# Optimization experiments

Hardware: AMD Instinct MI355X
Metric: run time of the kernel (lower is better)

The kernel has to match this reference:

```python
import jax, jax.numpy as jnp
import numpy as np

B, T, D, H, E = 4, 2048, 1024, 1024, 8
NEG_SLOPE = 0.01  # torch LeakyReLU default

def leaky_relu(x):
    return jnp.where(x >= 0, x, NEG_SLOPE * x)

def setup_inputs() -> dict:
    key = jax.random.key(0)
    ks = jax.random.split(key, 10)
    s = 0.02
    return {
        "x": jax.random.normal(ks[0], (B, T, D), jnp.float32),
        "gate_w": jax.random.normal(ks[1], (D, E), jnp.float32) * s,
        "gate_b": jnp.zeros((E,), jnp.float32),
        "w1": jax.random.normal(ks[2], (E, D, H), jnp.float32) * s,
        "b1": jnp.zeros((E, H), jnp.float32),
        "w2": jax.random.normal(ks[3], (E, H, H), jnp.float32) * s,
        "b2": jnp.zeros((E, H), jnp.float32),
        "w3": jax.random.normal(ks[4], (E, H, D), jnp.float32) * s,
        "b3": jnp.zeros((E, D), jnp.float32),
        "topn": 2,
    }

def reference(x, gate_w, gate_b, w1, b1, w2, b2, w3, b3, topn):
    # Gating: softmax over experts, top-k mask, L1 renormalize
    gating = jax.nn.softmax(x @ gate_w + gate_b, axis=-1)          # [B,T,E]
    _, topk_idx = jax.lax.top_k(gating, topn)                       # [B,T,k]
    mask = jax.nn.one_hot(topk_idx, E, dtype=gating.dtype).sum(-2)  # [B,T,E]
    g = gating * mask
    g = g / jnp.maximum(jnp.sum(jnp.abs(g), axis=-1, keepdims=True), 1e-12)
    # Dense all-expert MLP: Linear -> LeakyReLU -> Linear -> LeakyReLU -> Linear
    h = leaky_relu(jnp.einsum('btd,edh->bteh', x, w1) + b1)         # [B,T,E,H]
    h = leaky_relu(jnp.einsum('bteh,ehg->bteg', h, w2) + b2)        # [B,T,E,H]
    eo = jnp.einsum('bteh,ehd->bted', h, w3) + b3                   # [B,T,E,D]
    # Weighted combine
    return jnp.einsum('bte,bted->btd', g, eo)                       # [B,T,D]
```

## Files before the change

kernel.cpp:

```cpp
#include <hip/hip_runtime.h>
#include <hip/hip_bf16.h>
#include <stdint.h>

#define TOKENS   8192
#define DDIM     1024
#define EXPERTS  8
#define NSLOT    (TOKENS * 2)
#define MAXTILE  136

typedef __bf16 bf16x8_t __attribute__((ext_vector_type(8)));
typedef __bf16 bf16x4_t __attribute__((ext_vector_type(4)));
typedef float  f32x4_t  __attribute__((ext_vector_type(4)));

__device__ __forceinline__ void gl_lds16(const void* g, void* l) {
  __builtin_amdgcn_global_load_lds(
      (const __attribute__((address_space(1))) void*)g,
      (__attribute__((address_space(3))) void*)l, 16, 0, 0);
}

__global__ void twt_k(const float* __restrict__ w1, const float* __restrict__ w2,
                      const float* __restrict__ w3, __bf16* __restrict__ w1T,
                      __bf16* __restrict__ w2T, __bf16* __restrict__ w3T) {
  __shared__ float tile[64][33];
  const int layer = blockIdx.z >> 3, e = blockIdx.z & 7;
  const float* w = (layer == 0) ? w1 : (layer == 1) ? w2 : w3;
  __bf16* wT = (layer == 0) ? w1T : (layer == 1) ? w2T : w3T;
  const int kb = blockIdx.x * 64, nb = blockIdx.y * 32;
  const size_t ebase = (size_t)e << 20;
  const int tx = threadIdx.x, ty = threadIdx.y;
  const float* src = w + ebase;
#pragma unroll
  for (int r = ty; r < 64; r += 8)
    tile[r][tx] = src[(size_t)(kb + r) * 1024 + nb + tx];
  __syncthreads();
  __bf16* dst = wT + ebase;
#pragma unroll
  for (int r = ty; r < 32; r += 8) {
    union { __bf16 h[2]; unsigned u; } pk;
    pk.h[0] = (__bf16)tile[2 * tx][r];
    pk.h[1] = (__bf16)tile[2 * tx + 1][r];
    *(unsigned*)(dst + (size_t)(nb + r) * 1024 + kb + 2 * tx) = pk.u;
  }
}

__global__ __launch_bounds__(256) void gate_k(
    const float* __restrict__ x, const float* __restrict__ gw,
    const float* __restrict__ gb, __bf16* __restrict__ xbf,
    int* __restrict__ top_i, float* __restrict__ top_w) {
  const int t = blockIdx.x * 4 + (threadIdx.x >> 6);
  const int lane = threadIdx.x & 63;
  const float4* x4 = (const float4*)(x + (size_t)t * DDIM);
  bf16x4_t* xo4 = (bf16x4_t*)(xbf + (size_t)t * DDIM);
  const float4* g4 = (const float4*)gw;
  float acc[EXPERTS];
#pragma unroll
  for (int e = 0; e < EXPERTS; ++e) acc[e] = 0.f;
#pragma unroll
  for (int d4 = lane; d4 < 256; d4 += 64) {
    const float4 v = x4[d4];
    bf16x4_t o = {(__bf16)v.x, (__bf16)v.y, (__bf16)v.z, (__bf16)v.w};
    xo4[d4] = o;
    const float4* g = g4 + (size_t)d4 * 8;
    float4 ga, gbv;
    ga = g[0]; gbv = g[1];
    acc[0] += v.x * ga.x; acc[1] += v.x * ga.y; acc[2] += v.x * ga.z; acc[3] += v.x * ga.w;
    acc[4] += v.x * gbv.x; acc[5] += v.x * gbv.y; acc[6] += v.x * gbv.z; acc[7] += v.x * gbv.w;
    ga = g[2]; gbv = g[3];
    acc[0] += v.y * ga.x; acc[1] += v.y * ga.y; acc[2] += v.y * ga.z; acc[3] += v.y * ga.w;
    acc[4] += v.y * gbv.x; acc[5] += v.y * gbv.y; acc[6] += v.y * gbv.z; acc[7] += v.y * gbv.w;
    ga = g[4]; gbv = g[5];
    acc[0] += v.z * ga.x; acc[1] += v.z * ga.y; acc[2] += v.z * ga.z; acc[3] += v.z * ga.w;
    acc[4] += v.z * gbv.x; acc[5] += v.z * gbv.y; acc[6] += v.z * gbv.z; acc[7] += v.z * gbv.w;
    ga = g[6]; gbv = g[7];
    acc[0] += v.w * ga.x; acc[1] += v.w * ga.y; acc[2] += v.w * ga.z; acc[3] += v.w * ga.w;
    acc[4] += v.w * gbv.x; acc[5] += v.w * gbv.y; acc[6] += v.w * gbv.z; acc[7] += v.w * gbv.w;
  }
#pragma unroll
  for (int e = 0; e < EXPERTS; ++e)
    for (int s = 32; s > 0; s >>= 1) acc[e] += __shfl_down(acc[e], s);
  if (lane == 0) {
#pragma unroll
    for (int e = 0; e < EXPERTS; ++e) acc[e] += gb[e];
    int i1 = 0;
    for (int e = 1; e < EXPERTS; ++e)
      if (acc[e] > acc[i1]) i1 = e;
    int i2 = (i1 == 0) ? 1 : 0;
    for (int e = 0; e < EXPERTS; ++e)
      if (e != i1 && acc[e] > acc[i2]) i2 = e;
    const float r = expf(acc[i2] - acc[i1]);
    const float wA = 1.f / (1.f + r);
    const float wB = r / (1.f + r);
    top_i[t * 2] = i1; top_i[t * 2 + 1] = i2;
    top_w[t * 2] = wA; top_w[t * 2 + 1] = wB;
  }
}

__global__ __launch_bounds__(1024) void plan_k(
    const int* __restrict__ top_i, int* __restrict__ eoff,
    int* __restrict__ tok_list, int* __restrict__ slot_of,
    int4* __restrict__ work, int* __restrict__ ntiles) {
  const int tid = threadIdx.x;
  const int lane = tid & 63, wid = tid >> 6;
  __shared__ int ws[16][EXPERTS];
  __shared__ int eoff_s[EXPERTS];
  __shared__ int base_lds[1024 * EXPERTS];

  int ids[16];
  unsigned long long h64 = 0;
#pragma unroll
  for (int j = 0; j < 16; ++j) {
    ids[j] = top_i[tid * 16 + j];
    h64 += 1ull << (ids[j] * 8);
  }
#pragma unroll
  for (int e = 0; e < EXPERTS; ++e) {
    const int h = (int)((h64 >> (8 * e)) & 0xff);
    int v = h;
    for (int s = 1; s < 64; s <<= 1) {
      const int u = __shfl_up(v, s);
      if (lane >= s) v += u;
    }
    const int excl = v - h;
    const int tot = __shfl(v, 63);
    if (lane == 0) ws[wid][e] = tot;
    base_lds[tid * EXPERTS + e] = excl;
  }
  __syncthreads();
  if (tid == 0) {
    int tot[EXPERTS];
    for (int e = 0; e < EXPERTS; ++e) {
      int run = 0;
      for (int w = 0; w < 16; ++w) { const int c = ws[w][e]; ws[w][e] = run; run += c; }
      tot[e] = run;
    }
    int s = 0, nt = 0;
    for (int e = 0; e < EXPERTS; ++e) {
      const int te = tot[e];
      eoff_s[e] = s; eoff[e] = s;
      const int mt = (te + 127) >> 7;
      for (int i = 0; i < mt; ++i) { work[nt] = make_int4(e, i << 7, s, te); ++nt; }
      s += te;
    }
    eoff[EXPERTS] = s;
    ntiles[0] = nt;
  }
  __syncthreads();
#pragma unroll
  for (int e = 0; e < EXPERTS; ++e)
    base_lds[tid * EXPERTS + e] += eoff_s[e] + ws[wid][e];
  unsigned long long pre64 = 0;
#pragma unroll
  for (int j = 0; j < 16; ++j) {
    const int entry = tid * 16 + j;
    const int e = ids[j];
    const int pre = (int)((pre64 >> (8 * e)) & 0xff);
    pre64 += 1ull << (8 * e);
    const int s = base_lds[tid * EXPERTS + e] + pre;
    tok_list[s] = entry >> 1;
    slot_of[entry] = s;
  }
}

template <int GATHER, int LEAKY>
__global__ __launch_bounds__(256) void moe_gemm(
    const __bf16* __restrict__ A, const int* __restrict__ tok,
    const __bf16* __restrict__ W, const float* __restrict__ bias,
    const int4* __restrict__ work, const int* __restrict__ ntiles,
    __bf16* __restrict__ out) {
  if ((int)blockIdx.y >= ntiles[0]) return;
  const int4 wk = work[blockIdx.y];
  const int e = wk.x;
  const int m0 = wk.y;
  const int off = wk.z;
  const int ne = wk.w;
  const int n0 = blockIdx.x * 128;

  __shared__ __align__(16) __bf16 As[3][128 * 32];
  __shared__ __align__(16) __bf16 Bs[3][128 * 32];

  const int tid = threadIdx.x;
  const int lane = tid & 63;
  const int wid = tid >> 6;
  const int wm = wid >> 1, wn = wid & 1;
  const int ln = lane & 15, quad = lane >> 4;

  const __bf16* aptr[2];
  const __bf16* bptr[2];
#pragma unroll
  for (int j = 0; j < 2; ++j) {
    const int c = (wid * 2 + j) * 64 + lane;
    const int row = c >> 2;
    const int kc = (c & 3) ^ ((row >> 1) & 3);
    int r = m0 + row;
    if (r >= ne) r = m0;
    const long arow = GATHER ? (long)tok[off + r] : (long)(off + r);
    aptr[j] = A + arow * DDIM + kc * 8;
    bptr[j] = W + ((long)e << 20) + (long)(n0 + row) * 1024 + kc * 8;
  }
  const int st0 = (wid * 2) * 512;
  const int st1 = (wid * 2 + 1) * 512;

  const int swz = (quad ^ ((ln >> 1) & 3)) * 8;

  const f32x4_t vzero = {0.f, 0.f, 0.f, 0.f};
  f32x4_t acc[4][4];
#pragma unroll
  for (int i = 0; i < 4; ++i)
#pragma unroll
    for (int j = 0; j < 4; ++j) acc[i][j] = vzero;

#define STAGE(SB, KT)                                        \
  do {                                                       \
    const int k0_ = (KT) * 32;                               \
    gl_lds16(aptr[0] + k0_, (__bf16*)As[SB] + st0);          \
    gl_lds16(aptr[1] + k0_, (__bf16*)As[SB] + st1);          \
    gl_lds16(bptr[0] + k0_, (__bf16*)Bs[SB] + st0);          \
    gl_lds16(bptr[1] + k0_, (__bf16*)Bs[SB] + st1);          \
  } while (0)

#define WAITB(N)                                             \
  do {                                                       \
    asm volatile("s_waitcnt vmcnt(" #N ")" ::: "memory");    \
    __builtin_amdgcn_s_barrier();                            \
  } while (0)

#define COMPUTE(CUR)                                                        \
  do {                                                                      \
    bf16x8_t aF[4], bF[4];                                                  \
    _Pragma("unroll") for (int i = 0; i < 4; ++i)                           \
        aF[i] = *(const bf16x8_t*)(&As[CUR][(wm * 64 + i * 16 + ln) * 32 +  \
                                            swz]);                          \
    _Pragma("unroll") for (int j = 0; j < 4; ++j)                           \
        bF[j] = *(const bf16x8_t*)(&Bs[CUR][(wn * 64 + j * 16 + ln) * 32 +  \
                                            swz]);                          \
    _Pragma("unroll") for (int i = 0; i < 4; ++i)                           \
        _Pragma("unroll") for (int j = 0; j < 4; ++j)                       \
            acc[i][j] = __builtin_amdgcn_mfma_f32_16x16x32_bf16(            \
                bF[j], aF[i], acc[i][j], 0, 0, 0);                          \
  } while (0)

  STAGE(0, 0);
  STAGE(1, 1);

#pragma unroll 1
  for (int kt = 0; kt < 30; kt += 3) {
    WAITB(4); STAGE(2, kt + 2); COMPUTE(0);
    WAITB(4); STAGE(0, kt + 3); COMPUTE(1);
    WAITB(4); STAGE(1, kt + 4); COMPUTE(2);
  }
  WAITB(4); COMPUTE(0);
  WAITB(0); COMPUTE(1);

#undef STAGE
#undef WAITB
#undef COMPUTE

  const float* bs = bias + (e << 10);
  const int nb = n0 + wn * 64 + quad * 4;
  float4 bv[4];
#pragma unroll
  for (int j = 0; j < 4; ++j) bv[j] = *(const float4*)(bs + nb + j * 16);
#pragma unroll
  for (int i = 0; i < 4; ++i) {
    const int m = m0 + wm * 64 + i * 16 + ln;
    if (m < ne) {
      __bf16* orow = out + (size_t)(off + m) * 1024 + nb;
#pragma unroll
      for (int j = 0; j < 4; ++j) {
        float t0 = acc[i][j][0] + bv[j].x;
        float t1 = acc[i][j][1] + bv[j].y;
        float t2 = acc[i][j][2] + bv[j].z;
        float t3 = acc[i][j][3] + bv[j].w;
        if (LEAKY) {
          t0 = (t0 >= 0.f) ? t0 : 0.01f * t0;
          t1 = (t1 >= 0.f) ? t1 : 0.01f * t1;
          t2 = (t2 >= 0.f) ? t2 : 0.01f * t2;
          t3 = (t3 >= 0.f) ? t3 : 0.01f * t3;
        }
        bf16x4_t pk = {(__bf16)t0, (__bf16)t1, (__bf16)t2, (__bf16)t3};
        *(bf16x4_t*)(orow + j * 16) = pk;
      }
    }
  }
}

__global__ __launch_bounds__(256) void combine_k(
    const __bf16* __restrict__ eo, const int* __restrict__ slot_of,
    const float* __restrict__ top_w, float* __restrict__ out) {
  const int t = blockIdx.x;
  const int s1 = slot_of[t * 2], s2 = slot_of[t * 2 + 1];
  const float w1 = top_w[t * 2], w2 = top_w[t * 2 + 1];
  const bf16x4_t a = ((const bf16x4_t*)(eo + (size_t)s1 * DDIM))[threadIdx.x];
  const bf16x4_t b = ((const bf16x4_t*)(eo + (size_t)s2 * DDIM))[threadIdx.x];
  float4 o;
  o.x = w1 * (float)a[0] + w2 * (float)b[0];
  o.y = w1 * (float)a[1] + w2 * (float)b[1];
  o.z = w1 * (float)a[2] + w2 * (float)b[2];
  o.w = w1 * (float)a[3] + w2 * (float)b[3];
  ((float4*)(out + (size_t)t * DDIM))[threadIdx.x] = o;
}

extern "C" void kernel_launch(void* const* d_in, const int* in_sizes, int n_in,
                              void* d_out, int out_size, void* d_ws,
                              size_t ws_size, hipStream_t stream) {
  (void)in_sizes; (void)n_in; (void)out_size; (void)ws_size;
  const float* x  = (const float*)d_in[0];
  const float* gw = (const float*)d_in[1];
  const float* gb = (const float*)d_in[2];
  const float* w1 = (const float*)d_in[3];
  const float* b1 = (const float*)d_in[4];
  const float* w2 = (const float*)d_in[5];
  const float* b2 = (const float*)d_in[6];
  const float* w3 = (const float*)d_in[7];
  const float* b3 = (const float*)d_in[8];
  float* out = (float*)d_out;

  uint8_t* p = (uint8_t*)d_ws;
  auto alloc = [&](size_t b) {
    uint8_t* r = p;
    p += (b + 255) & ~(size_t)255;
    return r;
  };
  int*    eoff     = (int*)alloc(4 * (EXPERTS + 1));
  int*    ntiles   = (int*)alloc(4);
  int4*   work     = (int4*)alloc(16 * MAXTILE);
  int*    top_i    = (int*)alloc(4ull * TOKENS * 2);
  float*  top_w    = (float*)alloc(4ull * TOKENS * 2);
  int*    slot_of  = (int*)alloc(4ull * TOKENS * 2);
  int*    tok_list = (int*)alloc(4ull * NSLOT);
  __bf16* xbf      = (__bf16*)alloc(2ull * TOKENS * DDIM);
  __bf16* w1T      = (__bf16*)alloc(2ull * EXPERTS * 1024 * 1024);
  __bf16* w2T      = (__bf16*)alloc(2ull * EXPERTS * 1024 * 1024);
  __bf16* w3T      = (__bf16*)alloc(2ull * EXPERTS * 1024 * 1024);
  __bf16* h1       = (__bf16*)alloc(2ull * NSLOT * 1024);
  __bf16* h2       = (__bf16*)alloc(2ull * NSLOT * 1024);
  __bf16* eo       = (__bf16*)alloc(2ull * NSLOT * 1024);

  gate_k<<<TOKENS / 4, 256, 0, stream>>>(x, gw, gb, xbf, top_i, top_w);
  twt_k<<<dim3(16, 32, 24), dim3(32, 8), 0, stream>>>(w1, w2, w3, w1T, w2T, w3T);
  plan_k<<<1, 1024, 0, stream>>>(top_i, eoff, tok_list, slot_of, work, ntiles);

  moe_gemm<1, 1><<<dim3(8, MAXTILE), 256, 0, stream>>>(
      xbf, tok_list, w1T, b1, work, ntiles, h1);
  moe_gemm<0, 1><<<dim3(8, MAXTILE), 256, 0, stream>>>(
      h1, tok_list, w2T, b2, work, ntiles, h2);
  moe_gemm<0, 0><<<dim3(8, MAXTILE), 256, 0, stream>>>(
      h2, tok_list, w3T, b3, work, ntiles, eo);

  combine_k<<<TOKENS, 256, 0, stream>>>(eo, slot_of, top_w, out);
}
```

Measured before the change: 462.2 us.

## Widen MoE GEMM tile to 128x256 with 8 waves, retune transpose and combine

The grouped GEMM moves from 128x128 tiles with 256 threads to 128x256 tiles with 512 threads (8 waves, 2x4 wave grid). This halves redundant A-tile loads per output column and adjusts the async-load wait counts to match three loads per stage. The weight transpose kernel is rewritten to read float4 rows and write 16-byte bf16 vectors through a larger LDS tile. The combine kernel now processes four tokens per block with 8-wide bf16 loads. Larger tiles use more LDS and registers per block, which may reduce occupancy, and produce fewer blocks per expert tile row.

```diff
diff --git a/kernel.cpp b/kernel.cpp
--- a/kernel.cpp
+++ b/kernel.cpp
@@ -6,7 +6,7 @@
 #define DDIM     1024
 #define EXPERTS  8
 #define NSLOT    (TOKENS * 2)
-#define MAXTILE  136
+#define MAXT     136
 
 typedef __bf16 bf16x8_t __attribute__((ext_vector_type(8)));
 typedef __bf16 bf16x4_t __attribute__((ext_vector_type(4)));
@@ -18,28 +18,39 @@
       (__attribute__((address_space(3))) void*)l, 16, 0, 0);
 }
 
-__global__ void twt_k(const float* __restrict__ w1, const float* __restrict__ w2,
-                      const float* __restrict__ w3, __bf16* __restrict__ w1T,
-                      __bf16* __restrict__ w2T, __bf16* __restrict__ w3T) {
-  __shared__ float tile[64][33];
+__global__ __launch_bounds__(256) void twt_k(
+    const float* __restrict__ w1, const float* __restrict__ w2,
+    const float* __restrict__ w3, __bf16* __restrict__ w1T,
+    __bf16* __restrict__ w2T, __bf16* __restrict__ w3T) {
+  __shared__ __bf16 lt[64][264];
   const int layer = blockIdx.z >> 3, e = blockIdx.z & 7;
   const float* w = (layer == 0) ? w1 : (layer == 1) ? w2 : w3;
   __bf16* wT = (layer == 0) ? w1T : (layer == 1) ? w2T : w3T;
-  const int kb = blockIdx.x * 64, nb = blockIdx.y * 32;
   const size_t ebase = (size_t)e << 20;
-  const int tx = threadIdx.x, ty = threadIdx.y;
-  const float* src = w + ebase;
-#pragma unroll
-  for (int r = ty; r < 64; r += 8)
-    tile[r][tx] = src[(size_t)(kb + r) * 1024 + nb + tx];
+  const int kb = blockIdx.x * 256, nb = blockIdx.y * 64;
+  const int tid = threadIdx.x;
+  const float* src = w + ebase + (size_t)kb * 1024 + nb;
+  const int rr = tid >> 4;
+  const int c4 = tid & 15;
+#pragma unroll
+  for (int pass = 0; pass < 16; ++pass) {
+    const int k = pass * 16 + rr;
+    const float4 v = *(const float4*)(src + (size_t)k * 1024 + c4 * 4);
+    const int n = c4 * 4;
+    lt[n + 0][k] = (__bf16)v.x;
+    lt[n + 1][k] = (__bf16)v.y;
+    lt[n + 2][k] = (__bf16)v.z;
+    lt[n + 3][k] = (__bf16)v.w;
+  }
   __syncthreads();
-  __bf16* dst = wT + ebase;
-#pragma unroll
-  for (int r = ty; r < 32; r += 8) {
-    union { __bf16 h[2]; unsigned u; } pk;
-    pk.h[0] = (__bf16)tile[2 * tx][r];
-    pk.h[1] = (__bf16)tile[2 * tx + 1][r];
-    *(unsigned*)(dst + (size_t)(nb + r) * 1024 + kb + 2 * tx) = pk.u;
+  __bf16* dst = wT + ebase + (size_t)nb * 1024 + kb;
+  const int n8 = tid >> 5;
+  const int l16 = tid & 31;
+#pragma unroll
+  for (int pass = 0; pass < 8; ++pass) {
+    const int n = pass * 8 + n8;
+    const bf16x8_t v = *(const bf16x8_t*)(&lt[n][l16 * 8]);
+    *(bf16x8_t*)(dst + (size_t)n * 1024 + l16 * 8) = v;
   }
 }
 
@@ -162,7 +173,7 @@
 }
 
 template <int GATHER, int LEAKY>
-__global__ __launch_bounds__(256) void moe_gemm(
+__global__ __launch_bounds__(512, 4) void moe_gemm(
     const __bf16* __restrict__ A, const int* __restrict__ tok,
     const __bf16* __restrict__ W, const float* __restrict__ bias,
     const int4* __restrict__ work, const int* __restrict__ ntiles,
@@ -173,32 +184,35 @@
   const int m0 = wk.y;
   const int off = wk.z;
   const int ne = wk.w;
-  const int n0 = blockIdx.x * 128;
+  const int n0 = blockIdx.x * 256;
 
   __shared__ __align__(16) __bf16 As[3][128 * 32];
-  __shared__ __align__(16) __bf16 Bs[3][128 * 32];
+  __shared__ __align__(16) __bf16 Bs[3][256 * 32];
 
   const int tid = threadIdx.x;
   const int lane = tid & 63;
   const int wid = tid >> 6;
-  const int wm = wid >> 1, wn = wid & 1;
+  const int wm = wid >> 2, wn = wid & 3;
   const int ln = lane & 15, quad = lane >> 4;
 
-  const __bf16* aptr[2];
+  const int arow = tid >> 2;
+  const int kca = (tid & 3) ^ ((arow >> 1) & 3);
+  int ra = m0 + arow;
+  if (ra >= ne) ra = m0;
+  const long arowg = GATHER ? (long)tok[off + ra] : (long)(off + ra);
+  const __bf16* aptr = A + arowg * DDIM + kca * 8;
+  const int ast = wid * 512;
+
   const __bf16* bptr[2];
+  int bst[2];
 #pragma unroll
   for (int j = 0; j < 2; ++j) {
     const int c = (wid * 2 + j) * 64 + lane;
     const int row = c >> 2;
     const int kc = (c & 3) ^ ((row >> 1) & 3);
-    int r = m0 + row;
-    if (r >= ne) r = m0;
-    const long arow = GATHER ? (long)tok[off + r] : (long)(off + r);
-    aptr[j] = A + arow * DDIM + kc * 8;
     bptr[j] = W + ((long)e << 20) + (long)(n0 + row) * 1024 + kc * 8;
-  }
-  const int st0 = (wid * 2) * 512;
-  const int st1 = (wid * 2 + 1) * 512;
+    bst[j] = (wid * 2 + j) * 512;
+  }
 
   const int swz = (quad ^ ((ln >> 1) & 3)) * 8;
 
@@ -212,10 +226,9 @@
 #define STAGE(SB, KT)                                        \
   do {                                                       \
     const int k0_ = (KT) * 32;                               \
-    gl_lds16(aptr[0] + k0_, (__bf16*)As[SB] + st0);          \
-    gl_lds16(aptr[1] + k0_, (__bf16*)As[SB] + st1);          \
-    gl_lds16(bptr[0] + k0_, (__bf16*)Bs[SB] + st0);          \
-    gl_lds16(bptr[1] + k0_, (__bf16*)Bs[SB] + st1);          \
+    gl_lds16(aptr + k0_, (__bf16*)As[SB] + ast);             \
+    gl_lds16(bptr[0] + k0_, (__bf16*)Bs[SB] + bst[0]);       \
+    gl_lds16(bptr[1] + k0_, (__bf16*)Bs[SB] + bst[1]);       \
   } while (0)
 
 #define WAITB(N)                                             \
@@ -244,11 +257,11 @@
 
 #pragma unroll 1
   for (int kt = 0; kt < 30; kt += 3) {
-    WAITB(4); STAGE(2, kt + 2); COMPUTE(0);
-    WAITB(4); STAGE(0, kt + 3); COMPUTE(1);
-    WAITB(4); STAGE(1, kt + 4); COMPUTE(2);
-  }
-  WAITB(4); COMPUTE(0);
+    WAITB(3); STAGE(2, kt + 2); COMPUTE(0);
+    WAITB(3); STAGE(0, kt + 3); COMPUTE(1);
+    WAITB(3); STAGE(1, kt + 4); COMPUTE(2);
+  }
+  WAITB(3); COMPUTE(0);
   WAITB(0); COMPUTE(1);
 
 #undef STAGE
@@ -287,17 +300,30 @@
 __global__ __launch_bounds__(256) void combine_k(
     const __bf16* __restrict__ eo, const int* __restrict__ slot_of,
     const float* __restrict__ top_w, float* __restrict__ out) {
-  const int t = blockIdx.x;
+  const int t = blockIdx.x * 4 + (threadIdx.x >> 6);
+  const int lane = threadIdx.x & 63;
   const int s1 = slot_of[t * 2], s2 = slot_of[t * 2 + 1];
   const float w1 = top_w[t * 2], w2 = top_w[t * 2 + 1];
-  const bf16x4_t a = ((const bf16x4_t*)(eo + (size_t)s1 * DDIM))[threadIdx.x];
-  const bf16x4_t b = ((const bf16x4_t*)(eo + (size_t)s2 * DDIM))[threadIdx.x];
-  float4 o;
-  o.x = w1 * (float)a[0] + w2 * (float)b[0];
-  o.y = w1 * (float)a[1] + w2 * (float)b[1];
-  o.z = w1 * (float)a[2] + w2 * (float)b[2];
-  o.w = w1 * (float)a[3] + w2 * (float)b[3];
-  ((float4*)(out + (size_t)t * DDIM))[threadIdx.x] = o;
+  const bf16x8_t* r1 = (const bf16x8_t*)(eo + (size_t)s1 * DDIM);
+  const bf16x8_t* r2 = (const bf16x8_t*)(eo + (size_t)s2 * DDIM);
+  float4* o4 = (float4*)(out + (size_t)t * DDIM);
+#pragma unroll
+  for (int i = 0; i < 2; ++i) {
+    const int idx = lane * 2 + i;
+    const bf16x8_t a = r1[idx];
+    const bf16x8_t b = r2[idx];
+    float4 o0, o1;
+    o0.x = w1 * (float)a[0] + w2 * (float)b[0];
+    o0.y = w1 * (float)a[1] + w2 * (float)b[1];
+    o0.z = w1 * (float)a[2] + w2 * (float)b[2];
+    o0.w = w1 * (float)a[3] + w2 * (float)b[3];
+    o1.x = w1 * (float)a[4] + w2 * (float)b[4];
+    o1.y = w1 * (float)a[5] + w2 * (float)b[5];
+    o1.z = w1 * (float)a[6] + w2 * (float)b[6];
+    o1.w = w1 * (float)a[7] + w2 * (float)b[7];
+    o4[idx * 2] = o0;
+    o4[idx * 2 + 1] = o1;
+  }
 }
 
 extern "C" void kernel_launch(void* const* d_in, const int* in_sizes, int n_in,
@@ -323,7 +349,7 @@
   };
   int*    eoff     = (int*)alloc(4 * (EXPERTS + 1));
   int*    ntiles   = (int*)alloc(4);
-  int4*   work     = (int4*)alloc(16 * MAXTILE);
+  int4*   work     = (int4*)alloc(16 * MAXT);
   int*    top_i    = (int*)alloc(4ull * TOKENS * 2);
   float*  top_w    = (float*)alloc(4ull * TOKENS * 2);
   int*    slot_of  = (int*)alloc(4ull * TOKENS * 2);
@@ -337,15 +363,15 @@
   __bf16* eo       = (__bf16*)alloc(2ull * NSLOT * 1024);
 
   gate_k<<<TOKENS / 4, 256, 0, stream>>>(x, gw, gb, xbf, top_i, top_w);
-  twt_k<<<dim3(16, 32, 24), dim3(32, 8), 0, stream>>>(w1, w2, w3, w1T, w2T, w3T);
+  twt_k<<<dim3(4, 16, 24), 256, 0, stream>>>(w1, w2, w3, w1T, w2T, w3T);
   plan_k<<<1, 1024, 0, stream>>>(top_i, eoff, tok_list, slot_of, work, ntiles);
 
-  moe_gemm<1, 1><<<dim3(8, MAXTILE), 256, 0, stream>>>(
+  moe_gemm<1, 1><<<dim3(4, MAXT), 512, 0, stream>>>(
       xbf, tok_list, w1T, b1, work, ntiles, h1);
-  moe_gemm<0, 1><<<dim3(8, MAXTILE), 256, 0, stream>>>(
+  moe_gemm<0, 1><<<dim3(4, MAXT), 512, 0, stream>>>(
       h1, tok_list, w2T, b2, work, ntiles, h2);
-  moe_gemm<0, 0><<<dim3(8, MAXTILE), 256, 0, stream>>>(
+  moe_gemm<0, 0><<<dim3(4, MAXT), 512, 0, stream>>>(
       h2, tok_list, w3T, b3, work, ntiles, eo);
 
-  combine_k<<<TOKENS, 256, 0, stream>>>(eo, slot_of, top_w, out);
-}
+  combine_k<<<TOKENS / 4, 256, 0, stream>>>(eo, slot_of, top_w, out);
+}
```

After: 421.2 us. 1.1x faster.
